# Performance work log

Measured on AMD Instinct MI355X. Metric: run time of the kernel, lower is better.

## Reference

```python
import jax, jax.numpy as jnp
import numpy as np

B, C_IN, T = 256, 1024, 128   # batch, encoder channels, spectrogram frames (2**15 samples / 256 hop)
CTX, N_EVENTS = 64, 16        # context_dim, n_events (module constants)


def setup_inputs() -> dict:
    key = jax.random.key(0)
    k0, k1, k2 = jax.random.split(key, 3)
    return {
        "encoded": jax.random.normal(k0, (B, C_IN, T), dtype=jnp.float32),
        "w_vec": jax.random.normal(k1, (CTX, C_IN), dtype=jnp.float32) * 0.02,
        "b_vec": jnp.zeros((CTX,), dtype=jnp.float32),
        "w_switch": jax.random.normal(k2, (1, C_IN), dtype=jnp.float32) * 0.02,
        "b_switch": jnp.zeros((1,), dtype=jnp.float32),
    }


def reference(encoded, w_vec, b_vec, w_switch, b_switch):
    # 1x1 Conv1d == per-timestep matmul
    event_vecs = jnp.einsum('bct,dc->btd', encoded, w_vec) + b_vec          # [B,T,CTX]
    switch = jnp.einsum('bct,c->bt', encoded, w_switch[0]) + b_switch[0]    # [B,T]
    attn = jax.nn.relu(switch)                                              # [B,T]

    # sparsify: keep top-k attention values and their indices
    vals, idx = jax.lax.top_k(attn, N_EVENTS)                               # [B,K]

    # sparsify_vectors: gather event vectors at top-k time indices
    vecs = jnp.take_along_axis(event_vecs, idx[:, :, None], axis=1)         # [B,K,CTX]

    # scheduling[b, j, idx[b,j]] = attn[b, idx[b,j]] (vectorized scatter,
    # replaces the original nested python-loop scalar scatter)
    b_idx = jnp.arange(B)[:, None]
    j_idx = jnp.arange(N_EVENTS)[None, :]
    scheduling = jnp.zeros((B, N_EVENTS, T), dtype=attn.dtype)
    scheduling = scheduling.at[b_idx, j_idx, idx].set(vals)                 # [B,K,T]

    return vecs, scheduling
```

## Files before the change

### kernel.cpp

```cpp
#include <hip/hip_runtime.h>
#include <hip/hip_bf16.h>

#define C_IN 1024
#define T_SZ 128
#define CTX 64
#define NEV 16
#define BK 64
#define NTILE 16
#define NTHR 512
#define WROW 72
#define PLROW 132

typedef short bf16x8 __attribute__((ext_vector_type(8)));
typedef float f32x4 __attribute__((ext_vector_type(4)));

__device__ __forceinline__ unsigned short f2bf(float f) {
  __hip_bfloat16 h = __float2bfloat16(f);
  return *(unsigned short*)&h;
}

__global__ __launch_bounds__(NTHR, 1) void fused_sparsify(
    const float* __restrict__ enc,
    const float* __restrict__ wvec,
    const float* __restrict__ bvec,
    const float* __restrict__ wsw,
    const float* __restrict__ bsw,
    float* __restrict__ out)
{
  const int b    = blockIdx.x;
  const int tid  = threadIdx.x;
  const int lane = tid & 63;
  const int wv   = tid >> 6;
  const int g    = lane >> 4;
  const int tl   = lane & 15;
  const int n0   = wv * 16;

  __shared__ float encb[2][BK][T_SZ];
  __shared__ unsigned short Wb[2][CTX][WROW];
  __shared__ float wswl[C_IN];
  __shared__ float swpart[NTHR];
  __shared__ float attn[T_SZ];
  __shared__ float topv[NEV];
  __shared__ int   topi[NEV];

  const float* encB = enc + (size_t)b * (C_IN * T_SZ);

  wswl[tid]       = wsw[tid];
  wswl[tid + 512] = wsw[tid + 512];

  f32x4 acc0 = {0.f, 0.f, 0.f, 0.f};
  f32x4 acc1 = acc0, acc2 = acc0, acc3 = acc0;
  float sw_acc = 0.f;

  const int wd = tid >> 3;
  const int wc = (tid & 7) * 8;

  {
#pragma unroll
    for (int r = 0; r < 4; ++r) {
      int e = (r * NTHR + tid) * 4;
      __builtin_amdgcn_global_load_lds(
          (const __attribute__((address_space(1))) unsigned int*)(encB + e),
          (__attribute__((address_space(3))) unsigned int*)(&encb[0][0][0] + e),
          16, 0, 0);
    }
    float4 w0 = *(const float4*)(wvec + wd * C_IN + wc);
    float4 w1 = *(const float4*)(wvec + wd * C_IN + wc + 4);
    union { bf16x8 v; unsigned short u[8]; } pk;
    pk.u[0] = f2bf(w0.x); pk.u[1] = f2bf(w0.y); pk.u[2] = f2bf(w0.z); pk.u[3] = f2bf(w0.w);
    pk.u[4] = f2bf(w1.x); pk.u[5] = f2bf(w1.y); pk.u[6] = f2bf(w1.z); pk.u[7] = f2bf(w1.w);
    *(bf16x8*)&Wb[0][wd][wc] = pk.v;
  }
  __syncthreads();

  int cur = 0;
  for (int kt = 0; kt < NTILE; ++kt) {
    float4 wr0, wr1;
    const int nxt = cur ^ 1;
    if (kt + 1 < NTILE) {
      const float* gsrc = encB + (kt + 1) * (BK * T_SZ);
#pragma unroll
      for (int r = 0; r < 4; ++r) {
        int e = (r * NTHR + tid) * 4;
        __builtin_amdgcn_global_load_lds(
            (const __attribute__((address_space(1))) unsigned int*)(gsrc + e),
            (__attribute__((address_space(3))) unsigned int*)(&encb[nxt][0][0] + e),
            16, 0, 0);
      }
      wr0 = *(const float4*)(wvec + wd * C_IN + (kt + 1) * BK + wc);
      wr1 = *(const float4*)(wvec + wd * C_IN + (kt + 1) * BK + wc + 4);
    }

    const float* ec = &encb[cur][0][0];
    const unsigned short* Wc = &Wb[cur][0][0];
#pragma unroll
    for (int kk = 0; kk < BK; kk += 32) {
      union { bf16x8 v; unsigned short u[8]; } bu;
#pragma unroll
      for (int j = 0; j < 8; ++j)
        bu.u[j] = f2bf(ec[(kk + g * 8 + j) * T_SZ + n0 + tl]);
      bf16x8 a0 = *(const bf16x8*)&Wc[(0 * 16 + tl) * WROW + kk + g * 8];
      bf16x8 a1 = *(const bf16x8*)&Wc[(1 * 16 + tl) * WROW + kk + g * 8];
      bf16x8 a2 = *(const bf16x8*)&Wc[(2 * 16 + tl) * WROW + kk + g * 8];
      bf16x8 a3 = *(const bf16x8*)&Wc[(3 * 16 + tl) * WROW + kk + g * 8];
      acc0 = __builtin_amdgcn_mfma_f32_16x16x32_bf16(a0, bu.v, acc0, 0, 0, 0);
      acc1 = __builtin_amdgcn_mfma_f32_16x16x32_bf16(a1, bu.v, acc1, 0, 0, 0);
      acc2 = __builtin_amdgcn_mfma_f32_16x16x32_bf16(a2, bu.v, acc2, 0, 0, 0);
      acc3 = __builtin_amdgcn_mfma_f32_16x16x32_bf16(a3, bu.v, acc3, 0, 0, 0);
    }
    {
      const int tsw = tid & 127, cg = tid >> 7;
      const float* wst = wswl + kt * BK + cg * 16;
      const float* ep = ec + (cg * 16) * T_SZ + tsw;
      float s = 0.f;
#pragma unroll
      for (int c = 0; c < 16; ++c)
        s = fmaf(ep[c * T_SZ], wst[c], s);
      sw_acc += s;
    }

    if (kt + 1 < NTILE) {
      union { bf16x8 v; unsigned short u[8]; } pk;
      pk.u[0] = f2bf(wr0.x); pk.u[1] = f2bf(wr0.y); pk.u[2] = f2bf(wr0.z); pk.u[3] = f2bf(wr0.w);
      pk.u[4] = f2bf(wr1.x); pk.u[5] = f2bf(wr1.y); pk.u[6] = f2bf(wr1.z); pk.u[7] = f2bf(wr1.w);
      *(bf16x8*)&Wb[nxt][wd][wc] = pk.v;
    }
    __syncthreads();
    cur ^= 1;
  }

  swpart[tid] = sw_acc;
  __syncthreads();
  if (tid < T_SZ) {
    float s = swpart[tid] + swpart[tid + 128] + swpart[tid + 256] + swpart[tid + 384];
    s += bsw[0];
    attn[tid] = fmaxf(s, 0.f);
  }
  __syncthreads();

  if (tid < 64) {
    float v0 = attn[tid], v1 = attn[tid + 64];
#pragma unroll 1
    for (int r = 0; r < NEV; ++r) {
      float bv; int bi;
      if (v0 >= v1) { bv = v0; bi = tid; } else { bv = v1; bi = tid + 64; }
#pragma unroll
      for (int off = 32; off > 0; off >>= 1) {
        float ov = __shfl_xor(bv, off, 64);
        int   oi = __shfl_xor(bi, off, 64);
        if (ov > bv || (ov == bv && oi < bi)) { bv = ov; bi = oi; }
      }
      if (bi == tid) v0 = -__builtin_inff();
      if (bi == tid + 64) v1 = -__builtin_inff();
      if (tid == r) { topv[r] = bv; topi[r] = bi; }
    }
  }
  __syncthreads();

  float* Pl = (float*)&encb[0][0][0];
  {
#pragma unroll
    for (int r = 0; r < 4; ++r) {
      Pl[(0 * 16 + 4 * g + r) * PLROW + n0 + tl] = acc0[r];
      Pl[(1 * 16 + 4 * g + r) * PLROW + n0 + tl] = acc1[r];
      Pl[(2 * 16 + 4 * g + r) * PLROW + n0 + tl] = acc2[r];
      Pl[(3 * 16 + 4 * g + r) * PLROW + n0 + tl] = acc3[r];
    }
  }
  __syncthreads();

  {
    float* os = out + (256 * NEV * CTX) + b * (NEV * T_SZ);
    int j  = tid >> 5;
    int t0 = (tid * 4) & 127;
    float tv = topv[j];
    int   ti = topi[j];
    float4 v;
    v.x = (t0 + 0 == ti) ? tv : 0.f;
    v.y = (t0 + 1 == ti) ? tv : 0.f;
    v.z = (t0 + 2 == ti) ? tv : 0.f;
    v.w = (t0 + 3 == ti) ? tv : 0.f;
    *(float4*)&os[tid * 4] = v;
  }
  {
    float* ov = out + b * (NEV * CTX);
#pragma unroll
    for (int s = 0; s < 2; ++s) {
      int o = s * NTHR + tid;
      int j = o >> 6, d = o & 63;
      ov[o] = Pl[d * PLROW + topi[j]] + bvec[d];
    }
  }
}

extern "C" void kernel_launch(void* const* d_in, const int* in_sizes, int n_in,
                              void* d_out, int out_size, void* d_ws, size_t ws_size,
                              hipStream_t stream) {
  const float* enc  = (const float*)d_in[0];
  const float* wvec = (const float*)d_in[1];
  const float* bvec = (const float*)d_in[2];
  const float* wsw  = (const float*)d_in[3];
  const float* bsw  = (const float*)d_in[4];
  float* o = (float*)d_out;
  (void)in_sizes; (void)n_in; (void)out_size; (void)d_ws; (void)ws_size;
  fused_sparsify<<<256, NTHR, 0, stream>>>(enc, wvec, bvec, wsw, bsw, o);
}
```

Before: 38.11 us.

## Deepen encoder/weight prefetch to 4-stage async LDS pipeline with smaller K tiles

Replaces the double-buffered 64-wide K loop with a 4-buffer, 32-wide K pipeline. Encoder tiles are prefetched three steps ahead and weight tiles four steps ahead, both through global_load_lds, with manual vmcnt waits and raw s_barrier in place of __syncthreads. Weights now arrive in LDS as fp32 and are converted to bf16 one step ahead, instead of being loaded into registers. The goal is to hide more global-load latency for this single-block-per-batch kernel. The cost is twice as many barriers, more LDS use, and fragile hand-counted waitcnt logic.

```diff
diff --git a/kernel.cpp b/kernel.cpp
--- a/kernel.cpp
+++ b/kernel.cpp
@@ -5,10 +5,11 @@
 #define T_SZ 128
 #define CTX 64
 #define NEV 16
-#define BK 64
-#define NTILE 16
+#define BK 32
+#define NTILE 32
+#define NBUF 4
 #define NTHR 512
-#define WROW 72
+#define WBROW 40
 #define PLROW 132
 
 typedef short bf16x8 __attribute__((ext_vector_type(8)));
@@ -18,6 +19,17 @@
   __hip_bfloat16 h = __float2bfloat16(f);
   return *(unsigned short*)&h;
 }
+
+#define WAITVM(N) asm volatile("s_waitcnt vmcnt(" #N ")" ::: "memory")
+#define WAITLG()  asm volatile("s_waitcnt lgkmcnt(0)" ::: "memory")
+#define SCHED0()  __builtin_amdgcn_sched_barrier(0)
+
+#define GLD16(gp, lp) __builtin_amdgcn_global_load_lds( \
+    (const __attribute__((address_space(1))) unsigned int*)(gp), \
+    (__attribute__((address_space(3))) unsigned int*)(lp), 16, 0, 0)
+#define GLD4(gp, lp) __builtin_amdgcn_global_load_lds( \
+    (const __attribute__((address_space(1))) unsigned int*)(gp), \
+    (__attribute__((address_space(3))) unsigned int*)(lp), 4, 0, 0)
 
 __global__ __launch_bounds__(NTHR, 1) void fused_sparsify(
     const float* __restrict__ enc,
@@ -35,8 +47,9 @@
   const int tl   = lane & 15;
   const int n0   = wv * 16;
 
-  __shared__ float encb[2][BK][T_SZ];
-  __shared__ unsigned short Wb[2][CTX][WROW];
+  __shared__ float encb[NBUF][BK][T_SZ];
+  __shared__ float Wf[NBUF][CTX][BK];
+  __shared__ unsigned short Wbf[2][CTX][WBROW];
   __shared__ float wswl[C_IN];
   __shared__ float swpart[NTHR];
   __shared__ float attn[T_SZ];
@@ -45,64 +58,80 @@
 
   const float* encB = enc + (size_t)b * (C_IN * T_SZ);
 
-  wswl[tid]       = wsw[tid];
-  wswl[tid + 512] = wsw[tid + 512];
+  const int wd = tid >> 3;
+  const int wc = (tid & 7) * 4;
+
+  GLD4(wsw + tid,       &wswl[0] + tid);
+  GLD4(wsw + 512 + tid, &wswl[0] + 512 + tid);
+  GLD16(wvec + wd * C_IN + 0 * BK + wc, &Wf[0][0][0] + tid * 4);
+  GLD16(wvec + wd * C_IN + 1 * BK + wc, &Wf[1][0][0] + tid * 4);
+  {
+    int e0 = tid * 4, e1 = (512 + tid) * 4;
+    GLD16(encB + 0 * 4096 + e0, &encb[0][0][0] + e0);
+    GLD16(encB + 0 * 4096 + e1, &encb[0][0][0] + e1);
+    GLD16(wvec + wd * C_IN + 2 * BK + wc, &Wf[2][0][0] + tid * 4);
+    GLD16(encB + 1 * 4096 + e0, &encb[1][0][0] + e0);
+    GLD16(encB + 1 * 4096 + e1, &encb[1][0][0] + e1);
+    GLD16(wvec + wd * C_IN + 3 * BK + wc, &Wf[3][0][0] + tid * 4);
+    GLD16(encB + 2 * 4096 + e0, &encb[2][0][0] + e0);
+    GLD16(encB + 2 * 4096 + e1, &encb[2][0][0] + e1);
+  }
+  WAITVM(9);
+  SCHED0();
+  {
+    f32x4 w = *(const f32x4*)(&Wf[0][0][0] + tid * 4);
+    union { unsigned long long u; unsigned short s[4]; } pk;
+    pk.s[0] = f2bf(w[0]); pk.s[1] = f2bf(w[1]); pk.s[2] = f2bf(w[2]); pk.s[3] = f2bf(w[3]);
+    *(unsigned long long*)&Wbf[0][wd][wc] = pk.u;
+  }
+  WAITLG();
+  __builtin_amdgcn_s_barrier();
+  SCHED0();
 
   f32x4 acc0 = {0.f, 0.f, 0.f, 0.f};
   f32x4 acc1 = acc0, acc2 = acc0, acc3 = acc0;
   float sw_acc = 0.f;
 
-  const int wd = tid >> 3;
-  const int wc = (tid & 7) * 8;
-
-  {
-#pragma unroll
-    for (int r = 0; r < 4; ++r) {
-      int e = (r * NTHR + tid) * 4;
-      __builtin_amdgcn_global_load_lds(
-          (const __attribute__((address_space(1))) unsigned int*)(encB + e),
-          (__attribute__((address_space(3))) unsigned int*)(&encb[0][0][0] + e),
-          16, 0, 0);
-    }
-    float4 w0 = *(const float4*)(wvec + wd * C_IN + wc);
-    float4 w1 = *(const float4*)(wvec + wd * C_IN + wc + 4);
-    union { bf16x8 v; unsigned short u[8]; } pk;
-    pk.u[0] = f2bf(w0.x); pk.u[1] = f2bf(w0.y); pk.u[2] = f2bf(w0.z); pk.u[3] = f2bf(w0.w);
-    pk.u[4] = f2bf(w1.x); pk.u[5] = f2bf(w1.y); pk.u[6] = f2bf(w1.z); pk.u[7] = f2bf(w1.w);
-    *(bf16x8*)&Wb[0][wd][wc] = pk.v;
-  }
-  __syncthreads();
-
-  int cur = 0;
-  for (int kt = 0; kt < NTILE; ++kt) {
-    float4 wr0, wr1;
-    const int nxt = cur ^ 1;
-    if (kt + 1 < NTILE) {
-      const float* gsrc = encB + (kt + 1) * (BK * T_SZ);
-#pragma unroll
-      for (int r = 0; r < 4; ++r) {
-        int e = (r * NTHR + tid) * 4;
-        __builtin_amdgcn_global_load_lds(
-            (const __attribute__((address_space(1))) unsigned int*)(gsrc + e),
-            (__attribute__((address_space(3))) unsigned int*)(&encb[nxt][0][0] + e),
-            16, 0, 0);
-      }
-      wr0 = *(const float4*)(wvec + wd * C_IN + (kt + 1) * BK + wc);
-      wr1 = *(const float4*)(wvec + wd * C_IN + (kt + 1) * BK + wc + 4);
-    }
-
-    const float* ec = &encb[cur][0][0];
-    const unsigned short* Wc = &Wb[cur][0][0];
-#pragma unroll
-    for (int kk = 0; kk < BK; kk += 32) {
+#pragma unroll 1
+  for (int t = 0; t < NTILE; ++t) {
+    if (t < 29)      { WAITVM(6); }
+    else if (t == 29){ WAITVM(5); }
+    else if (t == 30){ WAITVM(2); }
+    else             { WAITVM(0); }
+    SCHED0();
+    WAITLG();
+    __builtin_amdgcn_s_barrier();
+    SCHED0();
+
+    if (t + 4 < NTILE) {
+      GLD16(wvec + wd * C_IN + (t + 4) * BK + wc, &Wf[(t + 4) & 3][0][0] + tid * 4);
+    }
+    if (t + 3 < NTILE) {
+      const float* gsrc = encB + (t + 3) * 4096;
+      float* ldst = &encb[(t + 3) & 3][0][0];
+      int e0 = tid * 4, e1 = (512 + tid) * 4;
+      GLD16(gsrc + e0, ldst + e0);
+      GLD16(gsrc + e1, ldst + e1);
+    }
+
+    if (t + 1 < NTILE) {
+      f32x4 w = *(const f32x4*)(&Wf[(t + 1) & 3][0][0] + tid * 4);
+      union { unsigned long long u; unsigned short s[4]; } pk;
+      pk.s[0] = f2bf(w[0]); pk.s[1] = f2bf(w[1]); pk.s[2] = f2bf(w[2]); pk.s[3] = f2bf(w[3]);
+      *(unsigned long long*)&Wbf[(t + 1) & 1][wd][wc] = pk.u;
+    }
+
+    const float* ec = &encb[t & 3][0][0];
+    const unsigned short* Wc = &Wbf[t & 1][0][0];
+    {
       union { bf16x8 v; unsigned short u[8]; } bu;
 #pragma unroll
       for (int j = 0; j < 8; ++j)
-        bu.u[j] = f2bf(ec[(kk + g * 8 + j) * T_SZ + n0 + tl]);
-      bf16x8 a0 = *(const bf16x8*)&Wc[(0 * 16 + tl) * WROW + kk + g * 8];
-      bf16x8 a1 = *(const bf16x8*)&Wc[(1 * 16 + tl) * WROW + kk + g * 8];
-      bf16x8 a2 = *(const bf16x8*)&Wc[(2 * 16 + tl) * WROW + kk + g * 8];
-      bf16x8 a3 = *(const bf16x8*)&Wc[(3 * 16 + tl) * WROW + kk + g * 8];
+        bu.u[j] = f2bf(ec[(g * 8 + j) * T_SZ + n0 + tl]);
+      bf16x8 a0 = *(const bf16x8*)&Wc[(0 * 16 + tl) * WBROW + g * 8];
+      bf16x8 a1 = *(const bf16x8*)&Wc[(1 * 16 + tl) * WBROW + g * 8];
+      bf16x8 a2 = *(const bf16x8*)&Wc[(2 * 16 + tl) * WBROW + g * 8];
+      bf16x8 a3 = *(const bf16x8*)&Wc[(3 * 16 + tl) * WBROW + g * 8];
       acc0 = __builtin_amdgcn_mfma_f32_16x16x32_bf16(a0, bu.v, acc0, 0, 0, 0);
       acc1 = __builtin_amdgcn_mfma_f32_16x16x32_bf16(a1, bu.v, acc1, 0, 0, 0);
       acc2 = __builtin_amdgcn_mfma_f32_16x16x32_bf16(a2, bu.v, acc2, 0, 0, 0);
@@ -110,23 +139,14 @@
     }
     {
       const int tsw = tid & 127, cg = tid >> 7;
-      const float* wst = wswl + kt * BK + cg * 16;
-      const float* ep = ec + (cg * 16) * T_SZ + tsw;
+      const float* wst = wswl + t * BK + cg * 8;
+      const float* ep = ec + (cg * 8) * T_SZ + tsw;
       float s = 0.f;
 #pragma unroll
-      for (int c = 0; c < 16; ++c)
+      for (int c = 0; c < 8; ++c)
         s = fmaf(ep[c * T_SZ], wst[c], s);
       sw_acc += s;
     }
-
-    if (kt + 1 < NTILE) {
-      union { bf16x8 v; unsigned short u[8]; } pk;
-      pk.u[0] = f2bf(wr0.x); pk.u[1] = f2bf(wr0.y); pk.u[2] = f2bf(wr0.z); pk.u[3] = f2bf(wr0.w);
-      pk.u[4] = f2bf(wr1.x); pk.u[5] = f2bf(wr1.y); pk.u[6] = f2bf(wr1.z); pk.u[7] = f2bf(wr1.w);
-      *(bf16x8*)&Wb[nxt][wd][wc] = pk.v;
-    }
-    __syncthreads();
-    cur ^= 1;
   }
 
   swpart[tid] = sw_acc;
```

Result: slower. 47.89 us (+25.7%).

## Register-staged pipeline with single bf16 conversion of encoder tiles

Applied to the files above, without the earlier changes.

Replaces the async global-to-LDS copy of fp32 encoder tiles with register-staged loads issued two tiles ahead. Each element is converted to bf16 once and stored transposed into a padded LDS buffer, instead of every wave converting fp32 from LDS inside the MFMA loop. The switch dot product is computed from the same registers during conversion. LDS use shrinks via a manual arena, and the accumulator spill is merged with the switch reduction to remove one barrier. The cost is higher register pressure and a barrier that waits only on lgkmcnt.

```diff
diff --git a/kernel.cpp b/kernel.cpp
--- a/kernel.cpp
+++ b/kernel.cpp
@@ -8,8 +8,17 @@
 #define BK 64
 #define NTILE 16
 #define NTHR 512
-#define WROW 72
+#define BROW 72
 #define PLROW 132
+
+#define BF_OFF 0
+#define WB_OFF 36864
+#define WS_OFF 55296
+#define SP_OFF 59392
+#define AT_OFF 63488
+#define TV_OFF 64000
+#define TI_OFF 64064
+#define ARENA_SZ 64128
 
 typedef short bf16x8 __attribute__((ext_vector_type(8)));
 typedef float f32x4 __attribute__((ext_vector_type(4)));
@@ -18,6 +27,52 @@
   __hip_bfloat16 h = __float2bfloat16(f);
   return *(unsigned short*)&h;
 }
+
+#define BARRIER() do { \
+  asm volatile("s_waitcnt lgkmcnt(0)" ::: "memory"); \
+  __builtin_amdgcn_s_barrier(); \
+} while (0)
+
+#define ISSUE(kt, ev, wv) do { \
+  const float* _s = encB + (kt) * (BK * T_SZ) + cb0 * T_SZ + t0; \
+  _Pragma("unroll") for (int _j = 0; _j < 8; ++_j) \
+    ev[_j] = *(const float2*)(_s + _j * T_SZ); \
+  const float* _w = wvec + wd * C_IN + (kt) * BK + wc; \
+  wv[0] = *(const float4*)_w; \
+  wv[1] = *(const float4*)(_w + 4); \
+} while (0)
+
+#define CONVERT(kt, ev, wv, buf) do { \
+  const float* _wt = wswl + (kt) * BK + cb0; \
+  union { bf16x8 v; unsigned short u[8]; } _p0, _p1, _pw; \
+  _Pragma("unroll") for (int _j = 0; _j < 8; ++_j) { \
+    sw0 = fmaf(ev[_j].x, _wt[_j], sw0); \
+    sw1 = fmaf(ev[_j].y, _wt[_j], sw1); \
+    _p0.u[_j] = f2bf(ev[_j].x); \
+    _p1.u[_j] = f2bf(ev[_j].y); \
+  } \
+  *(bf16x8*)&Bf[((buf) * T_SZ + t0) * BROW + cb0] = _p0.v; \
+  *(bf16x8*)&Bf[((buf) * T_SZ + t0 + 1) * BROW + cb0] = _p1.v; \
+  _pw.u[0] = f2bf(wv[0].x); _pw.u[1] = f2bf(wv[0].y); \
+  _pw.u[2] = f2bf(wv[0].z); _pw.u[3] = f2bf(wv[0].w); \
+  _pw.u[4] = f2bf(wv[1].x); _pw.u[5] = f2bf(wv[1].y); \
+  _pw.u[6] = f2bf(wv[1].z); _pw.u[7] = f2bf(wv[1].w); \
+  *(bf16x8*)&Wb[((buf) * CTX + wd) * BROW + wc] = _pw.v; \
+} while (0)
+
+#define MFMA_TILE(buf) do { \
+  _Pragma("unroll") for (int _ks = 0; _ks < 2; ++_ks) { \
+    bf16x8 _bv = *(const bf16x8*)&Bf[((buf) * T_SZ + n0 + tl) * BROW + _ks * 32 + g * 8]; \
+    bf16x8 _a0 = *(const bf16x8*)&Wb[((buf) * CTX +  0 + tl) * BROW + _ks * 32 + g * 8]; \
+    bf16x8 _a1 = *(const bf16x8*)&Wb[((buf) * CTX + 16 + tl) * BROW + _ks * 32 + g * 8]; \
+    bf16x8 _a2 = *(const bf16x8*)&Wb[((buf) * CTX + 32 + tl) * BROW + _ks * 32 + g * 8]; \
+    bf16x8 _a3 = *(const bf16x8*)&Wb[((buf) * CTX + 48 + tl) * BROW + _ks * 32 + g * 8]; \
+    acc0 = __builtin_amdgcn_mfma_f32_16x16x32_bf16(_a0, _bv, acc0, 0, 0, 0); \
+    acc1 = __builtin_amdgcn_mfma_f32_16x16x32_bf16(_a1, _bv, acc1, 0, 0, 0); \
+    acc2 = __builtin_amdgcn_mfma_f32_16x16x32_bf16(_a2, _bv, acc2, 0, 0, 0); \
+    acc3 = __builtin_amdgcn_mfma_f32_16x16x32_bf16(_a3, _bv, acc3, 0, 0, 0); \
+  } \
+} while (0)
 
 __global__ __launch_bounds__(NTHR, 1) void fused_sparsify(
     const float* __restrict__ enc,
@@ -30,18 +85,24 @@
   const int b    = blockIdx.x;
   const int tid  = threadIdx.x;
   const int lane = tid & 63;
-  const int wv   = tid >> 6;
+  const int wid  = tid >> 6;
   const int g    = lane >> 4;
   const int tl   = lane & 15;
-  const int n0   = wv * 16;
-
-  __shared__ float encb[2][BK][T_SZ];
-  __shared__ unsigned short Wb[2][CTX][WROW];
-  __shared__ float wswl[C_IN];
-  __shared__ float swpart[NTHR];
-  __shared__ float attn[T_SZ];
-  __shared__ float topv[NEV];
-  __shared__ int   topi[NEV];
+  const int n0   = wid * 16;
+
+  const int cb0 = wid * 8;
+  const int t0  = 2 * lane;
+  const int wd  = tid >> 3;
+  const int wc  = (tid & 7) * 8;
+
+  __shared__ __align__(16) char arena[ARENA_SZ];
+  unsigned short* Bf = (unsigned short*)(arena + BF_OFF);
+  unsigned short* Wb = (unsigned short*)(arena + WB_OFF);
+  float* wswl = (float*)(arena + WS_OFF);
+  float* swp  = (float*)(arena + SP_OFF);
+  float* attn = (float*)(arena + AT_OFF);
+  float* topv = (float*)(arena + TV_OFF);
+  int*   topi = (int*)(arena + TI_OFF);
 
   const float* encB = enc + (size_t)b * (C_IN * T_SZ);
 
@@ -50,91 +111,46 @@
 
   f32x4 acc0 = {0.f, 0.f, 0.f, 0.f};
   f32x4 acc1 = acc0, acc2 = acc0, acc3 = acc0;
-  float sw_acc = 0.f;
-
-  const int wd = tid >> 3;
-  const int wc = (tid & 7) * 8;
-
-  {
-#pragma unroll
-    for (int r = 0; r < 4; ++r) {
-      int e = (r * NTHR + tid) * 4;
-      __builtin_amdgcn_global_load_lds(
-          (const __attribute__((address_space(1))) unsigned int*)(encB + e),
-          (__attribute__((address_space(3))) unsigned int*)(&encb[0][0][0] + e),
-          16, 0, 0);
-    }
-    float4 w0 = *(const float4*)(wvec + wd * C_IN + wc);
-    float4 w1 = *(const float4*)(wvec + wd * C_IN + wc + 4);
-    union { bf16x8 v; unsigned short u[8]; } pk;
-    pk.u[0] = f2bf(w0.x); pk.u[1] = f2bf(w0.y); pk.u[2] = f2bf(w0.z); pk.u[3] = f2bf(w0.w);
-    pk.u[4] = f2bf(w1.x); pk.u[5] = f2bf(w1.y); pk.u[6] = f2bf(w1.z); pk.u[7] = f2bf(w1.w);
-    *(bf16x8*)&Wb[0][wd][wc] = pk.v;
-  }
+  float sw0 = 0.f, sw1 = 0.f;
+
+  float2 evA[8], evB[8];
+  float4 wvA[2], wvB[2];
+
+  ISSUE(0, evA, wvA);
+  ISSUE(1, evB, wvB);
+  BARRIER();
+  CONVERT(0, evA, wvA, 0);
+  BARRIER();
+
+#pragma unroll 1
+  for (int t = 0; t < NTILE; t += 2) {
+    if (t + 2 < NTILE) ISSUE(t + 2, evA, wvA);
+    MFMA_TILE(0);
+    CONVERT(t + 1, evB, wvB, 1);
+    BARRIER();
+    if (t + 3 < NTILE) ISSUE(t + 3, evB, wvB);
+    MFMA_TILE(1);
+    if (t + 2 < NTILE) CONVERT(t + 2, evA, wvA, 0);
+    BARRIER();
+  }
+
+  float* Pl = (float*)(arena + BF_OFF);
+#pragma unroll
+  for (int r = 0; r < 4; ++r) {
+    Pl[( 0 + 4 * g + r) * PLROW + n0 + tl] = acc0[r];
+    Pl[(16 + 4 * g + r) * PLROW + n0 + tl] = acc1[r];
+    Pl[(32 + 4 * g + r) * PLROW + n0 + tl] = acc2[r];
+    Pl[(48 + 4 * g + r) * PLROW + n0 + tl] = acc3[r];
+  }
+  swp[wid * T_SZ + t0]     = sw0;
+  swp[wid * T_SZ + t0 + 1] = sw1;
   __syncthreads();
 
-  int cur = 0;
-  for (int kt = 0; kt < NTILE; ++kt) {
-    float4 wr0, wr1;
-    const int nxt = cur ^ 1;
-    if (kt + 1 < NTILE) {
-      const float* gsrc = encB + (kt + 1) * (BK * T_SZ);
-#pragma unroll
-      for (int r = 0; r < 4; ++r) {
-        int e = (r * NTHR + tid) * 4;
-        __builtin_amdgcn_global_load_lds(
-            (const __attribute__((address_space(1))) unsigned int*)(gsrc + e),
-            (__attribute__((address_space(3))) unsigned int*)(&encb[nxt][0][0] + e),
-            16, 0, 0);
-      }
-      wr0 = *(const float4*)(wvec + wd * C_IN + (kt + 1) * BK + wc);
-      wr1 = *(const float4*)(wvec + wd * C_IN + (kt + 1) * BK + wc + 4);
-    }
-
-    const float* ec = &encb[cur][0][0];
-    const unsigned short* Wc = &Wb[cur][0][0];
-#pragma unroll
-    for (int kk = 0; kk < BK; kk += 32) {
-      union { bf16x8 v; unsigned short u[8]; } bu;
-#pragma unroll
-      for (int j = 0; j < 8; ++j)
-        bu.u[j] = f2bf(ec[(kk + g * 8 + j) * T_SZ + n0 + tl]);
-      bf16x8 a0 = *(const bf16x8*)&Wc[(0 * 16 + tl) * WROW + kk + g * 8];
-      bf16x8 a1 = *(const bf16x8*)&Wc[(1 * 16 + tl) * WROW + kk + g * 8];
-      bf16x8 a2 = *(const bf16x8*)&Wc[(2 * 16 + tl) * WROW + kk + g * 8];
-      bf16x8 a3 = *(const bf16x8*)&Wc[(3 * 16 + tl) * WROW + kk + g * 8];
-      acc0 = __builtin_amdgcn_mfma_f32_16x16x32_bf16(a0, bu.v, acc0, 0, 0, 0);
-      acc1 = __builtin_amdgcn_mfma_f32_16x16x32_bf16(a1, bu.v, acc1, 0, 0, 0);
-      acc2 = __builtin_amdgcn_mfma_f32_16x16x32_bf16(a2, bu.v, acc2, 0, 0, 0);
-      acc3 = __builtin_amdgcn_mfma_f32_16x16x32_bf16(a3, bu.v, acc3, 0, 0, 0);
-    }
-    {
-      const int tsw = tid & 127, cg = tid >> 7;
-      const float* wst = wswl + kt * BK + cg * 16;
-      const float* ep = ec + (cg * 16) * T_SZ + tsw;
-      float s = 0.f;
-#pragma unroll
-      for (int c = 0; c < 16; ++c)
-        s = fmaf(ep[c * T_SZ], wst[c], s);
-      sw_acc += s;
-    }
-
-    if (kt + 1 < NTILE) {
-      union { bf16x8 v; unsigned short u[8]; } pk;
-      pk.u[0] = f2bf(wr0.x); pk.u[1] = f2bf(wr0.y); pk.u[2] = f2bf(wr0.z); pk.u[3] = f2bf(wr0.w);
-      pk.u[4] = f2bf(wr1.x); pk.u[5] = f2bf(wr1.y); pk.u[6] = f2bf(wr1.z); pk.u[7] = f2bf(wr1.w);
-      *(bf16x8*)&Wb[nxt][wd][wc] = pk.v;
-    }
-    __syncthreads();
-    cur ^= 1;
-  }
-
-  swpart[tid] = sw_acc;
-  __syncthreads();
   if (tid < T_SZ) {
-    float s = swpart[tid] + swpart[tid + 128] + swpart[tid + 256] + swpart[tid + 384];
-    s += bsw[0];
-    attn[tid] = fmaxf(s, 0.f);
+    float s = 0.f;
+#pragma unroll
+    for (int k = 0; k < 8; ++k) s += swp[k * T_SZ + tid];
+    attn[tid] = fmaxf(s + bsw[0], 0.f);
   }
   __syncthreads();
 
@@ -157,29 +173,17 @@
   }
   __syncthreads();
 
-  float* Pl = (float*)&encb[0][0][0];
-  {
-#pragma unroll
-    for (int r = 0; r < 4; ++r) {
-      Pl[(0 * 16 + 4 * g + r) * PLROW + n0 + tl] = acc0[r];
-      Pl[(1 * 16 + 4 * g + r) * PLROW + n0 + tl] = acc1[r];
-      Pl[(2 * 16 + 4 * g + r) * PLROW + n0 + tl] = acc2[r];
-      Pl[(3 * 16 + 4 * g + r) * PLROW + n0 + tl] = acc3[r];
-    }
-  }
-  __syncthreads();
-
   {
     float* os = out + (256 * NEV * CTX) + b * (NEV * T_SZ);
     int j  = tid >> 5;
-    int t0 = (tid * 4) & 127;
+    int tt = (tid * 4) & 127;
     float tv = topv[j];
     int   ti = topi[j];
     float4 v;
-    v.x = (t0 + 0 == ti) ? tv : 0.f;
-    v.y = (t0 + 1 == ti) ? tv : 0.f;
-    v.z = (t0 + 2 == ti) ? tv : 0.f;
-    v.w = (t0 + 3 == ti) ? tv : 0.f;
+    v.x = (tt + 0 == ti) ? tv : 0.f;
+    v.y = (tt + 1 == ti) ? tv : 0.f;
+    v.z = (tt + 2 == ti) ? tv : 0.f;
+    v.w = (tt + 3 == ti) ? tv : 0.f;
     *(float4*)&os[tid * 4] = v;
   }
   {
```

Result: faster. 35.86 us (-5.9%).
